# Kernel optimization log

Hardware: AMD Instinct MI355X
Metric: run time of the kernel (lower is better)

The kernel has to match this reference:

```python
import jax, jax.numpy as jnp
import numpy as np

B, N, H, D, HID = 4, 1024, 16, 72, 1152
ATT = H * D

def setup_inputs() -> dict:
    key = jax.random.key(0)
    ks = jax.random.split(key, 5)
    s = 0.02
    return {
        "x": jax.random.normal(ks[0], (B, N, HID), dtype=jnp.float32),
        "w_qkv": jax.random.normal(ks[1], (HID, 3 * ATT), dtype=jnp.float32) * s,
        "b_qkv": jnp.zeros((3 * ATT,), dtype=jnp.float32),
        "w_out": jax.random.normal(ks[2], (ATT, HID), dtype=jnp.float32) * s,
        "b_out": jnp.zeros((HID,), dtype=jnp.float32),
    }

def reference(x, w_qkv, b_qkv, w_out, b_out):
    # QKV projection: [B,N,3*ATT]
    qkv = x @ w_qkv + b_qkv
    q, k, v = jnp.split(qkv, 3, axis=-1)
    # [B,N,H,D] -> [B,H,N,D]
    q = q.reshape(B, N, H, D).transpose(0, 2, 1, 3)
    k = k.reshape(B, N, H, D).transpose(0, 2, 1, 3)
    v = v.reshape(B, N, H, D).transpose(0, 2, 1, 3)
    scale = D ** -0.5
    att = jnp.einsum("bhqd,bhkd->bhqk", q, k) * scale
    att = jax.nn.softmax(att, axis=-1)
    out = jnp.einsum("bhqk,bhkd->bhqd", att, v)
    out = out.transpose(0, 2, 1, 3).reshape(B, N, ATT)
    return out @ w_out + b_out
```

## Files before the change

kernel.cpp:

```cpp
#include <hip/hip_runtime.h>
#include <cstdint>

#define NB 4
#define NSEQ 1024
#define NH 16
#define HD 72
#define HID 1152
#define QKV3 3456
#define DP 96
#define QSCALE 0.17003713711193175f

typedef __attribute__((ext_vector_type(8))) __bf16 bf16x8;
typedef __attribute__((ext_vector_type(4))) __bf16 bf16x4;
typedef __attribute__((ext_vector_type(4))) float f32x4;

#define AS1 __attribute__((address_space(1)))
#define AS3 __attribute__((address_space(3)))

__device__ __forceinline__ void gl_lds16(const void* g, void* l) {
    __builtin_amdgcn_global_load_lds((const AS1 uint32_t*)g, (AS3 uint32_t*)l, 16, 0, 0);
}

#define RAW_BAR() asm volatile("s_barrier" ::: "memory")

#define XB_OFF     0UL
#define WQKVT_OFF  9437184UL
#define WOUTT_OFF  17694720UL
#define QP_OFF     20643840UL
#define KP_OFF     33226752UL
#define VT_OFF     45809664UL


__global__ void pad_kernel(__bf16* __restrict__ Qp, __bf16* __restrict__ Kp,
                           __bf16* __restrict__ Vt) {
    int i = blockIdx.x * 256 + threadIdx.x;
    uint4 z = make_uint4(0u, 0u, 0u, 0u);
    if (i < 131072) {
        __bf16* base = (i & 65536) ? Kp : Qp;
        int row = i & 65535;
        uint4* p = (uint4*)(base + row * 96 + 72);
        p[0] = z; p[1] = z; p[2] = z;
    } else {
        int j = i - 131072;
        int bh = j / 1536, w = j - bh * 1536;
        *((uint4*)(Vt + (long)bh * 98304 + 73728) + w) = z;
    }
}

__global__ void conv_x_kernel(const float* __restrict__ in, __bf16* __restrict__ out, long n4) {
    long i = (long)blockIdx.x * blockDim.x + threadIdx.x;
    if (i >= n4) return;
    float4 v = ((const float4*)in)[i];
    bf16x4 o = { (__bf16)v.x, (__bf16)v.y, (__bf16)v.z, (__bf16)v.w };
    ((bf16x4*)out)[i] = o;
}

__global__ void transpose_cvt_kernel(const float* __restrict__ in, __bf16* __restrict__ out,
                                     int K, int Nc) {
    __shared__ float t[32][33];
    int n0 = blockIdx.x * 32, k0 = blockIdx.y * 32;
    int x = threadIdx.x, y = threadIdx.y;
    #pragma unroll
    for (int i = 0; i < 32; i += 8)
        t[y + i][x] = in[(long)(k0 + y + i) * Nc + n0 + x];
    __syncthreads();
    #pragma unroll
    for (int i = 0; i < 32; i += 8)
        out[(long)(n0 + y + i) * K + k0 + x] = (__bf16)t[x][y + i];
}


template<int MT>
__device__ __forceinline__ void gemm_core(
    const __bf16* __restrict__ A, const __bf16* __restrict__ Bt,
    int lda, int ldb, int ntk, long rowA0, long rowB0,
    char* lds, f32x4 acc[MT][4])
{
    constexpr int BM    = MT * 32;
    constexpr int ATILE = BM * 64;
    constexpr int TILE  = ATILE + 256 * 64;

    const int tid  = threadIdx.x;
    const int wave = tid >> 6, lane = tid & 63;
    const int wm = wave >> 2, wn = wave & 3;
    const int lhi = lane >> 4, llo = lane & 15;
    const int srow = tid >> 2;
    const int scol = (tid & 3) * 8;

    auto stage = [&](int kt, int buf) {
        char* base = lds + buf * TILE;
        #pragma unroll
        for (int j = 0; j < BM / 128; ++j) {
            int r  = srow + j * 128;
            int ks = scol ^ ((((unsigned)r >> 1) & 3) << 3);
            gl_lds16(A + (rowA0 + r) * (long)lda + kt * 32 + ks, base + tid * 16 + j * 8192);
        }
        #pragma unroll
        for (int j = 0; j < 2; ++j) {
            int r  = srow + j * 128;
            int ks = scol ^ ((((unsigned)r >> 1) & 3) << 3);
            gl_lds16(Bt + (rowB0 + r) * (long)ldb + kt * 32 + ks,
                     base + ATILE + tid * 16 + j * 8192);
        }
    };

    stage(0, 0);
    asm volatile("s_waitcnt vmcnt(0)" ::: "memory");
    RAW_BAR();

    #pragma unroll 1
    for (int t = 0; t < ntk; ++t) {
        char* Ab = lds + (t & 1) * TILE;
        char* Bb = Ab + ATILE;
        if (t + 1 < ntk) stage(t + 1, (t & 1) ^ 1);

        bf16x8 bfr[4];
        #pragma unroll
        for (int nt = 0; nt < 4; ++nt) {
            int R = wn * 64 + nt * 16 + llo;
            int b = (R * 64 + lhi * 16) ^ ((((unsigned)R >> 1) & 3) << 4);
            bfr[nt] = *(const bf16x8*)(Bb + b);
        }
        bf16x8 af[MT / 2];
        #pragma unroll
        for (int mt = 0; mt < MT / 2; ++mt) {
            int R = wm * (BM / 2) + mt * 16 + llo;
            int b = (R * 64 + lhi * 16) ^ ((((unsigned)R >> 1) & 3) << 4);
            af[mt] = *(const bf16x8*)(Ab + b);
        }
        __builtin_amdgcn_s_setprio(1);
        #pragma unroll
        for (int mt = 0; mt < MT / 2; ++mt)
            #pragma unroll
            for (int nt = 0; nt < 4; ++nt)
                acc[mt][nt] = __builtin_amdgcn_mfma_f32_16x16x32_bf16(af[mt], bfr[nt], acc[mt][nt], 0, 0, 0);
        __builtin_amdgcn_s_setprio(0);
        #pragma unroll
        for (int mt = 0; mt < MT / 2; ++mt) {
            int R = wm * (BM / 2) + (MT / 2 + mt) * 16 + llo;
            int b = (R * 64 + lhi * 16) ^ ((((unsigned)R >> 1) & 3) << 4);
            af[mt] = *(const bf16x8*)(Ab + b);
        }
        __builtin_amdgcn_s_setprio(1);
        #pragma unroll
        for (int mt = 0; mt < MT / 2; ++mt)
            #pragma unroll
            for (int nt = 0; nt < 4; ++nt)
                acc[MT / 2 + mt][nt] = __builtin_amdgcn_mfma_f32_16x16x32_bf16(af[mt], bfr[nt], acc[MT / 2 + mt][nt], 0, 0, 0);
        __builtin_amdgcn_s_setprio(0);
        asm volatile("s_waitcnt vmcnt(0)" ::: "memory");
        RAW_BAR();
    }
}


__global__ __launch_bounds__(512, 4) void gemm_qkv_kernel(
    const __bf16* __restrict__ xb, const __bf16* __restrict__ wqkvT,
    const float* __restrict__ b_qkv,
    __bf16* __restrict__ Qp, __bf16* __restrict__ Kp, __bf16* __restrict__ Vt)
{
    __shared__ char lds[49152];
    f32x4 acc[4][4];
    #pragma unroll
    for (int i = 0; i < 4; ++i)
        #pragma unroll
        for (int j = 0; j < 4; ++j) acc[i][j] = (f32x4){0.f, 0.f, 0.f, 0.f};

    int lin = blockIdx.x;
    int v   = (lin & 7) * 56 + (lin >> 3);
    int bx  = v / 14, by = v - bx * 14;
    long rowA0 = (long)bx * 128, rowB0 = (long)by * 256;

    gemm_core<4>(xb, wqkvT, HID, HID, HID / 32, rowA0, rowB0, lds, acc);

    const int wave = threadIdx.x >> 6, lane = threadIdx.x & 63;
    const int wm = wave >> 2, wn = wave & 3, lhi = lane >> 4, llo = lane & 15;

    #pragma unroll
    for (int nt = 0; nt < 4; ++nt) {
        int n = (int)rowB0 + wn * 64 + nt * 16 + llo;
        if (n >= QKV3) continue;
        int sec = n / HID;
        int nn  = n - sec * HID;
        int h   = nn / HD;
        int d   = nn - h * HD;
        float bias = b_qkv[n];
        if (sec == 2) {
            #pragma unroll
            for (int mt = 0; mt < 4; ++mt) {
                int m0 = (int)rowA0 + wm * 64 + mt * 16 + lhi * 4;
                int bb = m0 >> 10, nq0 = m0 & 1023;
                bf16x4 pk = { (__bf16)(acc[mt][nt][0] + bias), (__bf16)(acc[mt][nt][1] + bias),
                              (__bf16)(acc[mt][nt][2] + bias), (__bf16)(acc[mt][nt][3] + bias) };
                *(bf16x4*)(Vt + ((long)(bb * NH + h) * DP + d) * NSEQ + nq0) = pk;
            }
        } else {
            __bf16* dst = (sec == 0) ? Qp : Kp;
            float scl = (sec == 0) ? QSCALE : 1.0f;
            #pragma unroll
            for (int mt = 0; mt < 4; ++mt) {
                #pragma unroll
                for (int r = 0; r < 4; ++r) {
                    int m = (int)rowA0 + wm * 64 + mt * 16 + lhi * 4 + r;
                    int bb = m >> 10, nq = m & 1023;
                    long bhn = (long)(bb * NH + h) * NSEQ + nq;
                    dst[bhn * DP + d] = (__bf16)((acc[mt][nt][r] + bias) * scl);
                }
            }
        }
    }
}


__global__ __launch_bounds__(512, 4) void flash_kernel(
    const __bf16* __restrict__ Qp, const __bf16* __restrict__ Kp,
    const __bf16* __restrict__ Vt, __bf16* __restrict__ atto)
{
    __shared__ char lds[73728];
    const int tid  = threadIdx.x;
    const int wave = tid >> 6, lane = tid & 63;
    const int lhi = lane >> 4, llo = lane & 15;

    int lin = blockIdx.x;
    int v   = ((lin & 7) << 6) + (lin >> 3);
    const int qx = v & 7;
    const int bh = v >> 3;

    const __bf16* Qb  = Qp + (long)bh * NSEQ * DP;
    const char*   KbB = (const char*)(Kp + (long)bh * NSEQ * DP);
    const char*   VbB = (const char*)(Vt + (long)bh * DP * NSEQ);

    char* P = lds + 57344 + wave * 2048;
    const int q0 = qx * 128 + wave * 16;

    auto stageK = [&](int kt, int kbuf) {
        #pragma unroll
        for (int j = 0; j < 2; ++j) {
            int bk  = wave * 2 + j;
            int key = bk * 4 + (lane >> 4);
            int c   = (lane & 15) * 16;
            gl_lds16(KbB + ((long)(kt * 64 + key)) * 192 + (c ^ ((key & 7) << 4)),
                     lds + kbuf * 16384 + bk * 1024);
        }
    };
    auto stageV = [&](int kt, int vb) {
        int dv = wave * 8 + (lane >> 3);
        int c  = (lane & 7) * 16;
        gl_lds16(VbB + (long)dv * 2048 + kt * 128 + (c ^ ((dv & 7) << 4)),
                 lds + 32768 + vb * 12288 + wave * 1024);
        if (wave < 4) {
            int dv2 = 64 + wave * 8 + (lane >> 3);
            gl_lds16(VbB + (long)dv2 * 2048 + kt * 128 + (c ^ ((dv2 & 7) << 4)),
                     lds + 32768 + vb * 12288 + 8192 + wave * 1024);
        }
    };

    bf16x8 aq[3];
    #pragma unroll
    for (int dc = 0; dc < 3; ++dc)
        aq[dc] = *(const bf16x8*)(Qb + (long)(q0 + llo) * DP + dc * 32 + lhi * 8);

    float mr = -3.0e38f, lr = 0.f;
    f32x4 acc[5];
    #pragma unroll
    for (int t = 0; t < 5; ++t) acc[t] = (f32x4){0.f, 0.f, 0.f, 0.f};

    stageK(0, 0);
    stageV(0, 0);
    asm volatile("s_waitcnt vmcnt(0)" ::: "memory");
    RAW_BAR();

    #pragma unroll 1
    for (int kb = 0; kb < 16; ++kb) {
        const int buf = kb & 1;
        if (kb < 15) {
            stageK(kb + 1, buf ^ 1);
            stageV(kb + 1, buf ^ 1);
        }

        f32x4 s[4];
        __builtin_amdgcn_s_setprio(1);
        #pragma unroll
        for (int ct = 0; ct < 4; ++ct) {
            f32x4 z = (f32x4){0.f, 0.f, 0.f, 0.f};
            #pragma unroll
            for (int dc = 0; dc < 3; ++dc) {
                bf16x8 kf = *(const bf16x8*)(lds + buf * 16384 +
                    (((ct * 16 + llo) * 256 + dc * 64 + lhi * 16) ^ ((llo & 7) << 4)));
                z = __builtin_amdgcn_mfma_f32_16x16x32_bf16(kf, aq[dc], z, 0, 0, 0);
            }
            s[ct] = z;
        }
        __builtin_amdgcn_s_setprio(0);

        float m0 = fmaxf(fmaxf(s[0][0], s[0][1]), fmaxf(s[0][2], s[0][3]));
        float m1 = fmaxf(fmaxf(s[1][0], s[1][1]), fmaxf(s[1][2], s[1][3]));
        float m2 = fmaxf(fmaxf(s[2][0], s[2][1]), fmaxf(s[2][2], s[2][3]));
        float m3 = fmaxf(fmaxf(s[3][0], s[3][1]), fmaxf(s[3][2], s[3][3]));
        float mx = fmaxf(fmaxf(m0, m1), fmaxf(m2, m3));
        mx = fmaxf(mx, __shfl_xor(mx, 16, 64));
        mx = fmaxf(mx, __shfl_xor(mx, 32, 64));
        if (!__all(mx <= mr + 8.0f)) {
            float mn = fmaxf(mr, mx);
            float al = exp2f(mr - mn);
            mr = mn;
            lr *= al;
            #pragma unroll
            for (int t = 0; t < 5; ++t)
                #pragma unroll
                for (int r = 0; r < 4; ++r) acc[t][r] *= al;
        }
        float p[4][4]; float sm = 0.f;
        #pragma unroll
        for (int ct = 0; ct < 4; ++ct)
            #pragma unroll
            for (int r = 0; r < 4; ++r) { p[ct][r] = exp2f(s[ct][r] - mr); sm += p[ct][r]; }
        sm += __shfl_xor(sm, 16, 64);
        sm += __shfl_xor(sm, 32, 64);
        lr += sm;
        #pragma unroll
        for (int ct = 0; ct < 4; ++ct) {
            bf16x4 pk = { (__bf16)p[ct][0], (__bf16)p[ct][1], (__bf16)p[ct][2], (__bf16)p[ct][3] };
            *(bf16x4*)(P + ((llo * 128 + ct * 32 + lhi * 8) ^ ((llo & 7) << 4))) = pk;
        }
        asm volatile("s_waitcnt lgkmcnt(0)" ::: "memory");

        __builtin_amdgcn_s_setprio(1);
        #pragma unroll
        for (int nc = 0; nc < 2; ++nc) {
            bf16x8 pP = *(const bf16x8*)(P + ((llo * 128 + nc * 64 + lhi * 16) ^ ((llo & 7) << 4)));
            #pragma unroll
            for (int t = 0; t < 5; ++t) {
                bf16x8 bv = *(const bf16x8*)(lds + 32768 + buf * 12288 +
                    (((t * 16 + llo) * 128 + nc * 64 + lhi * 16) ^ ((llo & 7) << 4)));
                acc[t] = __builtin_amdgcn_mfma_f32_16x16x32_bf16(bv, pP, acc[t], 0, 0, 0);
            }
        }
        __builtin_amdgcn_s_setprio(0);

        if (kb < 15) asm volatile("s_waitcnt vmcnt(0)" ::: "memory");
        RAW_BAR();
    }

    const float linv = 1.f / lr;
    const int b = bh >> 4, h = bh & 15;
    const int q = q0 + llo;
    __bf16* outP = atto + (long)(b * NSEQ + q) * HID + h * HD;
    #pragma unroll
    for (int t = 0; t < 5; ++t) {
        int d0 = t * 16 + lhi * 4;
        if (d0 < HD) {
            bf16x4 o = { (__bf16)(acc[t][0] * linv), (__bf16)(acc[t][1] * linv),
                         (__bf16)(acc[t][2] * linv), (__bf16)(acc[t][3] * linv) };
            *(bf16x4*)(outP + d0) = o;
        }
    }
}


__global__ __launch_bounds__(512, 4) void gemm_out_kernel(
    const __bf16* __restrict__ atto, const __bf16* __restrict__ woutT,
    const float* __restrict__ b_out, float* __restrict__ out)
{
    __shared__ char lds[49152];
    f32x4 acc[4][4];
    #pragma unroll
    for (int i = 0; i < 4; ++i)
        #pragma unroll
        for (int j = 0; j < 4; ++j) acc[i][j] = (f32x4){0.f, 0.f, 0.f, 0.f};

    int lin = blockIdx.x;
    int v   = (lin & 7) * 20 + (lin >> 3);
    int bx  = v / 5, by = v - bx * 5;
    long rowA0 = (long)bx * 128, rowB0 = (long)by * 256;

    gemm_core<4>(atto, woutT, HID, HID, HID / 32, rowA0, rowB0, lds, acc);

    const int wave = threadIdx.x >> 6, lane = threadIdx.x & 63;
    const int wm = wave >> 2, wn = wave & 3, lhi = lane >> 4, llo = lane & 15;

    #pragma unroll
    for (int nt = 0; nt < 4; ++nt) {
        int n = (int)rowB0 + wn * 64 + nt * 16 + llo;
        if (n >= HID) continue;
        float bias = b_out[n];
        #pragma unroll
        for (int mt = 0; mt < 4; ++mt) {
            #pragma unroll
            for (int r = 0; r < 4; ++r) {
                int m = (int)rowA0 + wm * 64 + mt * 16 + lhi * 4 + r;
                out[(long)m * HID + n] = acc[mt][nt][r] + bias;
            }
        }
    }
}


extern "C" void kernel_launch(void* const* d_in, const int* in_sizes, int n_in,
                              void* d_out, int out_size, void* d_ws, size_t ws_size,
                              hipStream_t stream) {
    const float* x      = (const float*)d_in[0];
    const float* w_qkv  = (const float*)d_in[1];
    const float* b_qkv  = (const float*)d_in[2];
    const float* w_out  = (const float*)d_in[3];
    const float* b_out  = (const float*)d_in[4];
    float* out = (float*)d_out;
    char* ws = (char*)d_ws;

    __bf16* xb    = (__bf16*)(ws + XB_OFF);
    __bf16* atto  = (__bf16*)(ws + XB_OFF);
    __bf16* wqkvT = (__bf16*)(ws + WQKVT_OFF);
    __bf16* woutT = (__bf16*)(ws + WOUTT_OFF);
    __bf16* Qp    = (__bf16*)(ws + QP_OFF);
    __bf16* Kp    = (__bf16*)(ws + KP_OFF);
    __bf16* Vt    = (__bf16*)(ws + VT_OFF);

    pad_kernel<<<896, 256, 0, stream>>>(Qp, Kp, Vt);
    conv_x_kernel<<<4608, 256, 0, stream>>>(x, xb, 1179648L);
    transpose_cvt_kernel<<<dim3(108, 36), dim3(32, 8), 0, stream>>>(w_qkv, wqkvT, HID, QKV3);
    transpose_cvt_kernel<<<dim3(36, 36), dim3(32, 8), 0, stream>>>(w_out, woutT, HID, HID);
    gemm_qkv_kernel<<<448, 512, 0, stream>>>(xb, wqkvT, b_qkv, Qp, Kp, Vt);
    flash_kernel<<<512, 512, 0, stream>>>(Qp, Kp, Vt, atto);
    gemm_out_kernel<<<160, 512, 0, stream>>>(atto, woutT, b_out, out);
}
```

Before: 134.4 us.

## Merge prep kernels, triple-buffer GEMM loads, widen K-tile LDS swizzle

Four preprocessing launches (padding, x conversion, two weight transposes) are folded into one kernel that dispatches on block index, which removes launch gaps. The shared GEMM core moves from double to triple buffering, keeping two tiles of loads in flight with a partial vmcnt wait, and grows LDS to 72KB per block. The flash kernel's K-tile XOR swizzle widens from 3 to 4 bits to cut LDS bank conflicts. The larger LDS footprint may lower GEMM occupancy.

```diff
diff --git a/kernel.cpp b/kernel.cpp
--- a/kernel.cpp
+++ b/kernel.cpp
@@ -31,42 +31,49 @@
 #define VT_OFF     45809664UL
 
 
-__global__ void pad_kernel(__bf16* __restrict__ Qp, __bf16* __restrict__ Kp,
-                           __bf16* __restrict__ Vt) {
-    int i = blockIdx.x * 256 + threadIdx.x;
-    uint4 z = make_uint4(0u, 0u, 0u, 0u);
-    if (i < 131072) {
-        __bf16* base = (i & 65536) ? Kp : Qp;
-        int row = i & 65535;
-        uint4* p = (uint4*)(base + row * 96 + 72);
-        p[0] = z; p[1] = z; p[2] = z;
+__global__ void prep_kernel(const float* __restrict__ x, __bf16* __restrict__ xb,
+                            const float* __restrict__ w_qkv, __bf16* __restrict__ wqkvT,
+                            const float* __restrict__ w_out, __bf16* __restrict__ woutT,
+                            __bf16* __restrict__ Qp, __bf16* __restrict__ Kp,
+                            __bf16* __restrict__ Vt) {
+    __shared__ float t[32][33];
+    const int blk = blockIdx.x, tid = threadIdx.x;
+    if (blk < 4608) {
+        long i = (long)blk * 256 + tid;
+        float4 v = ((const float4*)x)[i];
+        bf16x4 o = { (__bf16)v.x, (__bf16)v.y, (__bf16)v.z, (__bf16)v.w };
+        ((bf16x4*)xb)[i] = o;
+    } else if (blk < 9792) {
+        const float* in;  __bf16* outp;  int Nc, K, n0, k0;
+        if (blk < 8496) {
+            int b = blk - 4608; in = w_qkv; outp = wqkvT; Nc = QKV3; K = HID;
+            n0 = (b % 108) * 32; k0 = (b / 108) * 32;
+        } else {
+            int b = blk - 8496; in = w_out; outp = woutT; Nc = HID; K = HID;
+            n0 = (b % 36) * 32; k0 = (b / 36) * 32;
+        }
+        int xx = tid & 31, yy = tid >> 5;
+        #pragma unroll
+        for (int i = 0; i < 32; i += 8)
+            t[yy + i][xx] = in[(long)(k0 + yy + i) * Nc + n0 + xx];
+        __syncthreads();
+        #pragma unroll
+        for (int i = 0; i < 32; i += 8)
+            outp[(long)(n0 + yy + i) * K + k0 + xx] = (__bf16)t[xx][yy + i];
     } else {
-        int j = i - 131072;
-        int bh = j / 1536, w = j - bh * 1536;
-        *((uint4*)(Vt + (long)bh * 98304 + 73728) + w) = z;
-    }
-}
-
-__global__ void conv_x_kernel(const float* __restrict__ in, __bf16* __restrict__ out, long n4) {
-    long i = (long)blockIdx.x * blockDim.x + threadIdx.x;
-    if (i >= n4) return;
-    float4 v = ((const float4*)in)[i];
-    bf16x4 o = { (__bf16)v.x, (__bf16)v.y, (__bf16)v.z, (__bf16)v.w };
-    ((bf16x4*)out)[i] = o;
-}
-
-__global__ void transpose_cvt_kernel(const float* __restrict__ in, __bf16* __restrict__ out,
-                                     int K, int Nc) {
-    __shared__ float t[32][33];
-    int n0 = blockIdx.x * 32, k0 = blockIdx.y * 32;
-    int x = threadIdx.x, y = threadIdx.y;
-    #pragma unroll
-    for (int i = 0; i < 32; i += 8)
-        t[y + i][x] = in[(long)(k0 + y + i) * Nc + n0 + x];
-    __syncthreads();
-    #pragma unroll
-    for (int i = 0; i < 32; i += 8)
-        out[(long)(n0 + y + i) * K + k0 + x] = (__bf16)t[x][y + i];
+        int i = (blk - 9792) * 256 + tid;
+        uint4 z = make_uint4(0u, 0u, 0u, 0u);
+        if (i < 131072) {
+            __bf16* base = (i & 65536) ? Kp : Qp;
+            int row = i & 65535;
+            uint4* p = (uint4*)(base + row * 96 + 72);
+            p[0] = z; p[1] = z; p[2] = z;
+        } else {
+            int j = i - 131072;
+            int bh = j / 1536, w = j - bh * 1536;
+            *((uint4*)(Vt + (long)bh * 98304 + 73728) + w) = z;
+        }
+    }
 }
 
 
@@ -79,6 +86,7 @@
     constexpr int BM    = MT * 32;
     constexpr int ATILE = BM * 64;
     constexpr int TILE  = ATILE + 256 * 64;
+    constexpr int L     = BM / 128 + 2;
 
     const int tid  = threadIdx.x;
     const int wave = tid >> 6, lane = tid & 63;
@@ -105,14 +113,17 @@
     };
 
     stage(0, 0);
-    asm volatile("s_waitcnt vmcnt(0)" ::: "memory");
+    stage(1, 1);
+    asm volatile("s_waitcnt vmcnt(%0)" :: "n"(L) : "memory");
     RAW_BAR();
 
+    int buf = 0;
     #pragma unroll 1
     for (int t = 0; t < ntk; ++t) {
-        char* Ab = lds + (t & 1) * TILE;
+        char* Ab = lds + buf * TILE;
         char* Bb = Ab + ATILE;
-        if (t + 1 < ntk) stage(t + 1, (t & 1) ^ 1);
+        int nb = buf + 2; if (nb >= 3) nb -= 3;
+        if (t + 2 < ntk) stage(t + 2, nb);
 
         bf16x8 bfr[4];
         #pragma unroll
@@ -148,8 +159,10 @@
             for (int nt = 0; nt < 4; ++nt)
                 acc[MT / 2 + mt][nt] = __builtin_amdgcn_mfma_f32_16x16x32_bf16(af[mt], bfr[nt], acc[MT / 2 + mt][nt], 0, 0, 0);
         __builtin_amdgcn_s_setprio(0);
-        asm volatile("s_waitcnt vmcnt(0)" ::: "memory");
+        if (t + 2 < ntk)      asm volatile("s_waitcnt vmcnt(%0)" :: "n"(L) : "memory");
+        else if (t + 1 < ntk) asm volatile("s_waitcnt vmcnt(0)" ::: "memory");
         RAW_BAR();
+        buf = (buf == 2) ? 0 : buf + 1;
     }
 }
 
@@ -159,7 +172,7 @@
     const float* __restrict__ b_qkv,
     __bf16* __restrict__ Qp, __bf16* __restrict__ Kp, __bf16* __restrict__ Vt)
 {
-    __shared__ char lds[49152];
+    __shared__ char lds[73728];
     f32x4 acc[4][4];
     #pragma unroll
     for (int i = 0; i < 4; ++i)
@@ -239,7 +252,7 @@
             int bk  = wave * 2 + j;
             int key = bk * 4 + (lane >> 4);
             int c   = (lane & 15) * 16;
-            gl_lds16(KbB + ((long)(kt * 64 + key)) * 192 + (c ^ ((key & 7) << 4)),
+            gl_lds16(KbB + ((long)(kt * 64 + key)) * 192 + (c ^ ((key & 15) << 4)),
                      lds + kbuf * 16384 + bk * 1024);
         }
     };
@@ -286,7 +299,7 @@
             #pragma unroll
             for (int dc = 0; dc < 3; ++dc) {
                 bf16x8 kf = *(const bf16x8*)(lds + buf * 16384 +
-                    (((ct * 16 + llo) * 256 + dc * 64 + lhi * 16) ^ ((llo & 7) << 4)));
+                    (((ct * 16 + llo) * 256 + dc * 64 + lhi * 16) ^ ((llo & 15) << 4)));
                 z = __builtin_amdgcn_mfma_f32_16x16x32_bf16(kf, aq[dc], z, 0, 0, 0);
             }
             s[ct] = z;
@@ -362,7 +375,7 @@
     const __bf16* __restrict__ atto, const __bf16* __restrict__ woutT,
     const float* __restrict__ b_out, float* __restrict__ out)
 {
-    __shared__ char lds[49152];
+    __shared__ char lds[73728];
     f32x4 acc[4][4];
     #pragma unroll
     for (int i = 0; i < 4; ++i)
@@ -415,10 +428,7 @@
     __bf16* Kp    = (__bf16*)(ws + KP_OFF);
     __bf16* Vt    = (__bf16*)(ws + VT_OFF);
 
-    pad_kernel<<<896, 256, 0, stream>>>(Qp, Kp, Vt);
-    conv_x_kernel<<<4608, 256, 0, stream>>>(x, xb, 1179648L);
-    transpose_cvt_kernel<<<dim3(108, 36), dim3(32, 8), 0, stream>>>(w_qkv, wqkvT, HID, QKV3);
-    transpose_cvt_kernel<<<dim3(36, 36), dim3(32, 8), 0, stream>>>(w_out, woutT, HID, HID);
+    prep_kernel<<<10688, 256, 0, stream>>>(x, xb, w_qkv, wqkvT, w_out, woutT, Qp, Kp, Vt);
     gemm_qkv_kernel<<<448, 512, 0, stream>>>(xb, wqkvT, b_qkv, Qp, Kp, Vt);
     flash_kernel<<<512, 512, 0, stream>>>(Qp, Kp, Vt, atto);
     gemm_out_kernel<<<160, 512, 0, stream>>>(atto, woutT, b_out, out);
```

Result: faster. 127.2 us (-5.4%).
